# Optimization experiments

Hardware: AMD Instinct MI355X
Metric: run time of the kernel (lower is better)

The kernel has to match this reference:

```python
import jax, jax.numpy as jnp
import numpy as np

N = 50000      # nodes
E = 800000     # edges (before self-loops)
F_IN = 128     # num_features
HID = 32       # hidden_channels
HEADS = 4
CLS = 40       # num_classes
NEG_SLOPE = 0.2


def setup_inputs() -> dict:
    key = jax.random.key(0)
    ks = jax.random.split(key, 10)
    s = 0.1
    x = jax.random.normal(ks[0], (N, F_IN), jnp.float32)
    edge_index = jax.random.randint(ks[1], (2, E), 0, N, jnp.int32)
    W1 = jax.random.normal(ks[2], (F_IN, HEADS * HID), jnp.float32) * s
    att_src1 = jax.random.normal(ks[3], (HEADS, HID), jnp.float32) * s
    att_dst1 = jax.random.normal(ks[4], (HEADS, HID), jnp.float32) * s
    b1 = jnp.zeros((HEADS * HID,), jnp.float32)
    W2 = jax.random.normal(ks[5], (HEADS * HID, CLS), jnp.float32) * s
    att_src2 = jax.random.normal(ks[6], (1, CLS), jnp.float32) * s
    att_dst2 = jax.random.normal(ks[7], (1, CLS), jnp.float32) * s
    b2 = jnp.zeros((CLS,), jnp.float32)
    return {"x": x, "edge_index": edge_index,
            "W1": W1, "att_src1": att_src1, "att_dst1": att_dst1, "b1": b1,
            "W2": W2, "att_src2": att_src2, "att_dst2": att_dst2, "b2": b2}


def gat_layer(x, src, dst, W, a_src, a_dst, b, concat):
    """PyG GATConv: per-head linear, edge attention logits a_src.h_j + a_dst.h_i,
    LeakyReLU, segment softmax over incoming edges per dst, weighted scatter-sum."""
    n = x.shape[0]
    H, C = a_src.shape
    h = (x @ W).reshape(n, H, C)                       # [N, H, C]
    al_s = jnp.einsum('nhc,hc->nh', h, a_src)          # [N, H]
    al_d = jnp.einsum('nhc,hc->nh', h, a_dst)          # [N, H]
    e = jax.nn.leaky_relu(al_s[src] + al_d[dst], NEG_SLOPE)  # [E, H]
    e_max = jax.lax.stop_gradient(jax.ops.segment_max(e, dst, num_segments=n))
    e = jnp.exp(e - e_max[dst])
    denom = jax.ops.segment_sum(e, dst, num_segments=n)      # [N, H]
    alpha = e / (denom[dst] + 1e-16)                         # [E, H]
    out = jax.ops.segment_sum(h[src] * alpha[:, :, None], dst, num_segments=n)  # [N, H, C]
    out = out.reshape(n, H * C) if concat else out.mean(axis=1)
    return out + b


def reference(x, edge_index, W1, att_src1, att_dst1, b1, W2, att_src2, att_dst2, b2):
    n = x.shape[0]
    loops = jnp.arange(n, dtype=edge_index.dtype)
    src = jnp.concatenate([edge_index[0], loops])  # PyG adds self-loops by default
    dst = jnp.concatenate([edge_index[1], loops])
    h = gat_layer(x, src, dst, W1, att_src1, att_dst1, b1, concat=True)
    h = jax.nn.relu(h)  # dropout is identity in eval mode
    h = gat_layer(h, src, dst, W2, att_src2, att_dst2, b2, concat=False)
    return jax.nn.log_softmax(h, axis=1)
```

## Files before the change

kernel.cpp:

```cpp
#include <hip/hip_runtime.h>
#include <hip/hip_bf16.h>
#include <cstdint>
#include <cstddef>

#define NN 50000
#define EE 800000
#define ETOT (EE + NN)
#define FIN 128
#define D1 128
#define HEADS 4
#define HID 32
#define CLS 40
#define NEG 0.2f
#define MAXDEG 64
#define NPART 8
#define PSIZE 6250
#define GB 104
#define BGB (NPART * GB)

typedef __attribute__((ext_vector_type(8))) short short8;
typedef __attribute__((ext_vector_type(4))) float float4v;

union U16 { uint4 u; short8 s; };

__device__ __forceinline__ float bf2f(unsigned short u) {
    union { unsigned int i; float f; } v; v.i = ((unsigned int)u) << 16; return v.f;
}
__device__ __forceinline__ unsigned short f2bf(float f) {
    union { unsigned int i; float f; } v; v.f = f;
    unsigned int r = v.i + 0x7fffu + ((v.i >> 16) & 1u);
    return (unsigned short)(r >> 16);
}

__global__ __launch_bounds__(256, 4) void bg_k(const int* __restrict__ eidx,
                                               int* __restrict__ cnt,
                                               unsigned short* __restrict__ ssrcp,
                                               const float* __restrict__ X,
                                               const float* __restrict__ W,
                                               const float* __restrict__ as1,
                                               const float* __restrict__ ad1,
                                               unsigned int* __restrict__ H1b,
                                               float* __restrict__ ALS1,
                                               float* __restrict__ ALD1) {
    __shared__ uint4 Wl[2048];
    __shared__ float sas[128], sad[128];
    int t = threadIdx.x;

    if (blockIdx.x < BGB) {
        int part = blockIdx.x & (NPART - 1);
        int g    = blockIdx.x >> 3;
        int lo = part * PSIZE, hi = lo + PSIZE;
        int stride = GB * 256;
        for (int i = g * 256 + t; i < ETOT; i += stride) {
            int dN = (i < EE) ? eidx[EE + i] : (i - EE);
            if (dN >= lo && dN < hi) {
                int sN = (i < EE) ? eidx[i] : dN;
                int slot = atomicAdd(&cnt[dN], 1);
                if (slot < MAXDEG) ssrcp[dN * MAXDEG + slot] = (unsigned short)sN;
            }
        }
        return;
    }

    int bI = blockIdx.x - BGB;
    if (t < 128) { sas[t] = as1[t]; sad[t] = ad1[t]; }
    for (int g = t; g < 2048; g += 256) {
        int ct = g >> 8, rem = g & 255, kc = rem >> 6, l = rem & 63;
        int c = ct * 16 + (l & 15);
        int k0 = kc * 32 + (l >> 4) * 8;
        U16 u;
#pragma unroll
        for (int j = 0; j < 8; j++) u.s[j] = (short)f2bf(W[(k0 + j) * D1 + c]);
        Wl[g] = u.u;
    }
    __syncthreads();

    int wid = t >> 6, lane = t & 63, quad = lane >> 4, lrow = lane & 15;
    int wrow0 = bI * 128 + wid * 32;

    short8 afr[2][4];
#pragma unroll
    for (int rt = 0; rt < 2; rt++) {
        int r = wrow0 + rt * 16 + lrow;
#pragma unroll
        for (int kc = 0; kc < 4; kc++) {
            short8 a = {0, 0, 0, 0, 0, 0, 0, 0};
            if (r < NN) {
                const float* xp = X + (size_t)r * FIN + kc * 32 + quad * 8;
                float4 x0 = *(const float4*)xp;
                float4 x1 = *(const float4*)(xp + 4);
                a[0] = (short)f2bf(x0.x); a[1] = (short)f2bf(x0.y);
                a[2] = (short)f2bf(x0.z); a[3] = (short)f2bf(x0.w);
                a[4] = (short)f2bf(x1.x); a[5] = (short)f2bf(x1.y);
                a[6] = (short)f2bf(x1.z); a[7] = (short)f2bf(x1.w);
            }
            afr[rt][kc] = a;
        }
    }

    float4v acc[2][4];

    for (int cp = 0; cp < 2; ++cp) {
#pragma unroll
        for (int rt = 0; rt < 2; rt++)
#pragma unroll
            for (int c4 = 0; c4 < 4; c4++) acc[rt][c4] = (float4v)(0.f);

#pragma unroll
        for (int c4 = 0; c4 < 4; c4++) {
#pragma unroll
            for (int kc = 0; kc < 4; kc++) {
                U16 b; b.u = Wl[((cp * 4 + c4) * 4 + kc) * 64 + lane];
                acc[0][c4] = __builtin_amdgcn_mfma_f32_16x16x32_bf16(afr[0][kc], b.s, acc[0][c4], 0, 0, 0);
                acc[1][c4] = __builtin_amdgcn_mfma_f32_16x16x32_bf16(afr[1][kc], b.s, acc[1][c4], 0, 0, 0);
            }
        }

#pragma unroll
        for (int rt = 0; rt < 2; rt++) {
#pragma unroll
            for (int reg = 0; reg < 4; reg++) {
                float ps[2] = {0.f, 0.f};
                float pd[2] = {0.f, 0.f};
#pragma unroll
                for (int c4 = 0; c4 < 4; c4++) {
                    float v = acc[rt][c4][reg];
                    int ct = cp * 4 + c4;
                    ps[c4 >> 1] += v * sas[ct * 16 + lrow];
                    pd[c4 >> 1] += v * sad[ct * 16 + lrow];
                }
#pragma unroll
                for (int o = 1; o < 16; o <<= 1) {
#pragma unroll
                    for (int h = 0; h < 2; h++) {
                        ps[h] += __shfl_xor(ps[h], o);
                        pd[h] += __shfl_xor(pd[h], o);
                    }
                }
                int r = wrow0 + rt * 16 + quad * 4 + reg;
                if (lrow == 0 && r < NN) {
                    *(float2*)&ALS1[(size_t)r * 4 + cp * 2] = make_float2(ps[0], ps[1]);
                    *(float2*)&ALD1[(size_t)r * 4 + cp * 2] = make_float2(pd[0], pd[1]);
                }
            }
        }

#pragma unroll
        for (int rt = 0; rt < 2; rt++)
#pragma unroll
            for (int c4 = 0; c4 < 4; c4++)
#pragma unroll
                for (int reg = 0; reg < 4; reg++) {
                    float v = acc[rt][c4][reg];
                    float o = __shfl_xor(v, 1);
                    int r = wrow0 + rt * 16 + quad * 4 + reg;
                    if (((lane & 1) == 0) && r < NN) {
                        unsigned int u = (unsigned int)f2bf(v) | ((unsigned int)f2bf(o) << 16);
                        H1b[(size_t)r * 64 + (cp * 4 + c4) * 8 + (lrow >> 1)] = u;
                    }
                }
    }
}

__global__ __launch_bounds__(256) void gather1_k(const int* __restrict__ cnt,
                                                 const unsigned short* __restrict__ ssrcp,
                                                 const uint4* __restrict__ H1b4,
                                                 const float4* __restrict__ ALS,
                                                 const float4* __restrict__ ALD,
                                                 const float* __restrict__ b1,
                                                 uint4* __restrict__ OUT1b4) {
    __shared__ float wlds[4][MAXDEG][4];
    __shared__ int sidlds[4][MAXDEG];
    int wid = threadIdx.x >> 6, lane = threadIdx.x & 63;
    int v = blockIdx.x * 4 + wid;
    int deg = min(cnt[v], MAXDEG);
    float4 ad = ALD[v];
    float w0 = 0.f, w1 = 0.f, w2 = 0.f, w3 = 0.f;
    if (lane < deg) {
        int s = (int)ssrcp[v * MAXDEG + lane];
        sidlds[wid][lane] = s;
        float4 as = ALS[s];
        float l0 = as.x + ad.x; l0 = l0 > 0.f ? l0 : NEG * l0;
        float l1 = as.y + ad.y; l1 = l1 > 0.f ? l1 : NEG * l1;
        float l2 = as.z + ad.z; l2 = l2 > 0.f ? l2 : NEG * l2;
        float l3 = as.w + ad.w; l3 = l3 > 0.f ? l3 : NEG * l3;
        w0 = __expf(l0); w1 = __expf(l1); w2 = __expf(l2); w3 = __expf(l3);
        wlds[wid][lane][0] = w0; wlds[wid][lane][1] = w1;
        wlds[wid][lane][2] = w2; wlds[wid][lane][3] = w3;
    }
    float d0 = w0, d1 = w1, d2 = w2, d3 = w3;
#pragma unroll
    for (int o = 1; o < 64; o <<= 1) {
        d0 += __shfl_xor(d0, o); d1 += __shfl_xor(d1, o);
        d2 += __shfl_xor(d2, o); d3 += __shfl_xor(d3, o);
    }
    __syncthreads();
    int g = lane >> 4, l = lane & 15, head = l >> 2;
    float a0=0.f,a1=0.f,a2=0.f,a3=0.f,a4=0.f,a5=0.f,a6=0.f,a7=0.f;
    for (int j = g; j < deg; j += 4) {
        float wj = wlds[wid][j][head];
        int s = sidlds[wid][j];
        uint4 q = H1b4[(size_t)s * 16 + l];
        a0 += wj * bf2f((unsigned short)(q.x & 0xffffu));
        a1 += wj * bf2f((unsigned short)(q.x >> 16));
        a2 += wj * bf2f((unsigned short)(q.y & 0xffffu));
        a3 += wj * bf2f((unsigned short)(q.y >> 16));
        a4 += wj * bf2f((unsigned short)(q.z & 0xffffu));
        a5 += wj * bf2f((unsigned short)(q.z >> 16));
        a6 += wj * bf2f((unsigned short)(q.w & 0xffffu));
        a7 += wj * bf2f((unsigned short)(q.w >> 16));
    }
#pragma unroll
    for (int o = 16; o < 64; o <<= 1) {
        a0 += __shfl_xor(a0, o); a1 += __shfl_xor(a1, o);
        a2 += __shfl_xor(a2, o); a3 += __shfl_xor(a3, o);
        a4 += __shfl_xor(a4, o); a5 += __shfl_xor(a5, o);
        a6 += __shfl_xor(a6, o); a7 += __shfl_xor(a7, o);
    }
    if (lane < 16) {
        float den = (head == 0) ? d0 : (head == 1) ? d1 : (head == 2) ? d2 : d3;
        den += 1e-16f;
        float4 bA = *(const float4*)&b1[8 * l];
        float4 bB = *(const float4*)&b1[8 * l + 4];
        float o0 = fmaxf(a0 / den + bA.x, 0.f);
        float o1 = fmaxf(a1 / den + bA.y, 0.f);
        float o2 = fmaxf(a2 / den + bA.z, 0.f);
        float o3 = fmaxf(a3 / den + bA.w, 0.f);
        float o4 = fmaxf(a4 / den + bB.x, 0.f);
        float o5 = fmaxf(a5 / den + bB.y, 0.f);
        float o6 = fmaxf(a6 / den + bB.z, 0.f);
        float o7 = fmaxf(a7 / den + bB.w, 0.f);
        uint4 u;
        u.x = (unsigned int)f2bf(o0) | ((unsigned int)f2bf(o1) << 16);
        u.y = (unsigned int)f2bf(o2) | ((unsigned int)f2bf(o3) << 16);
        u.z = (unsigned int)f2bf(o4) | ((unsigned int)f2bf(o5) << 16);
        u.w = (unsigned int)f2bf(o6) | ((unsigned int)f2bf(o7) << 16);
        OUT1b4[(size_t)v * 16 + l] = u;
    }
}

__global__ __launch_bounds__(256) void gemm2_k(const unsigned int* __restrict__ OUT1b,
                                               const float* __restrict__ W2,
                                               const float* __restrict__ as2,
                                               const float* __restrict__ ad2,
                                               unsigned int* __restrict__ H2b,
                                               float* __restrict__ ALS2,
                                               float* __restrict__ ALD2) {
    __shared__ uint4 Wl[768];
    __shared__ float sas[48], sad[48];
    int t = threadIdx.x;
    if (t < 48) {
        sas[t] = (t < CLS) ? as2[t] : 0.f;
        sad[t] = (t < CLS) ? ad2[t] : 0.f;
    }
    for (int g = t; g < 768; g += 256) {
        int ct = g >> 8, rem = g & 255, kc = rem >> 6, l = rem & 63;
        int c = ct * 16 + (l & 15);
        int k0 = kc * 32 + (l >> 4) * 8;
        U16 u;
#pragma unroll
        for (int j = 0; j < 8; j++)
            u.s[j] = (c < CLS) ? (short)f2bf(W2[(k0 + j) * CLS + c]) : (short)0;
        Wl[g] = u.u;
    }
    __syncthreads();

    int wid = t >> 6, lane = t & 63, quad = lane >> 4, lrow = lane & 15;
    int wrow0 = blockIdx.x * 128 + wid * 32;

    U16 afr[2][4];
#pragma unroll
    for (int rt = 0; rt < 2; rt++) {
        int r = wrow0 + rt * 16 + lrow;
#pragma unroll
        for (int kc = 0; kc < 4; kc++) {
            if (r < NN)
                afr[rt][kc].u = ((const uint4*)OUT1b)[(size_t)r * 16 + kc * 4 + quad];
            else
                afr[rt][kc].u = make_uint4(0, 0, 0, 0);
        }
    }

    float4v acc[2][3];
#pragma unroll
    for (int rt = 0; rt < 2; rt++)
#pragma unroll
        for (int ct = 0; ct < 3; ct++) acc[rt][ct] = (float4v)(0.f);

#pragma unroll
    for (int ct = 0; ct < 3; ct++) {
#pragma unroll
        for (int kc = 0; kc < 4; kc++) {
            U16 b; b.u = Wl[(ct * 4 + kc) * 64 + lane];
            acc[0][ct] = __builtin_amdgcn_mfma_f32_16x16x32_bf16(afr[0][kc].s, b.s, acc[0][ct], 0, 0, 0);
            acc[1][ct] = __builtin_amdgcn_mfma_f32_16x16x32_bf16(afr[1][kc].s, b.s, acc[1][ct], 0, 0, 0);
        }
    }

#pragma unroll
    for (int rt = 0; rt < 2; rt++) {
#pragma unroll
        for (int reg = 0; reg < 4; reg++) {
            float ps = 0.f, pd = 0.f;
#pragma unroll
            for (int ct = 0; ct < 3; ct++) {
                float v = acc[rt][ct][reg];
                ps += v * sas[ct * 16 + lrow];
                pd += v * sad[ct * 16 + lrow];
            }
#pragma unroll
            for (int o = 1; o < 16; o <<= 1) {
                ps += __shfl_xor(ps, o);
                pd += __shfl_xor(pd, o);
            }
            int r = wrow0 + rt * 16 + quad * 4 + reg;
            if (lrow == 0 && r < NN) {
                ALS2[r] = ps;
                ALD2[r] = pd;
            }
        }
    }

#pragma unroll
    for (int rt = 0; rt < 2; rt++)
#pragma unroll
        for (int ct = 0; ct < 3; ct++)
#pragma unroll
            for (int reg = 0; reg < 4; reg++) {
                float v = acc[rt][ct][reg];
                float o = __shfl_xor(v, 1);
                int r = wrow0 + rt * 16 + quad * 4 + reg;
                int c = ct * 16 + lrow;
                if (((lane & 1) == 0) && c < CLS && r < NN) {
                    unsigned int u = (unsigned int)f2bf(v) | ((unsigned int)f2bf(o) << 16);
                    H2b[(size_t)r * 20 + (c >> 1)] = u;
                }
            }
}

__global__ __launch_bounds__(256) void gather2_k(const int* __restrict__ cnt,
                                                 const unsigned short* __restrict__ ssrcp,
                                                 const unsigned int* __restrict__ H2b,
                                                 const float* __restrict__ ALS,
                                                 const float* __restrict__ ALD,
                                                 const float* __restrict__ b2,
                                                 float* __restrict__ out) {
    int wid = threadIdx.x >> 6, t = threadIdx.x & 63;
    int v = blockIdx.x * 4 + wid;
    int deg = min(cnt[v], MAXDEG);
    __shared__ float w[4][MAXDEG];
    __shared__ int sid[4][MAXDEG];
    __shared__ float part[4][2][CLS];
    float den = 0.f;
    float adv = ALD[v];
    if (t < deg) {
        int s = (int)ssrcp[(size_t)v * MAXDEG + t];
        sid[wid][t] = s;
        float l = ALS[s] + adv; l = l > 0.f ? l : NEG * l;
        float e = __expf(l);
        w[wid][t] = e; den = e;
    }
    __syncthreads();
    int g = t >> 5, c = t & 31;
    if (c < 20) {
        float ax = 0.f, ay = 0.f;
        for (int j = g; j < deg; j += 2) {
            float wj = w[wid][j];
            unsigned int u = H2b[(size_t)sid[wid][j] * 20 + c];
            ax += wj * bf2f((unsigned short)(u & 0xffffu));
            ay += wj * bf2f((unsigned short)(u >> 16));
        }
        part[wid][g][2 * c] = ax;
        part[wid][g][2 * c + 1] = ay;
    }
#pragma unroll
    for (int o = 32; o > 0; o >>= 1) den += __shfl_xor(den, o);
    __syncthreads();
    float z = (t < CLS) ? (part[wid][0][t] + part[wid][1][t]) / (den + 1e-16f) + b2[t] : -1e30f;
    float mx = z;
#pragma unroll
    for (int o = 32; o > 0; o >>= 1) mx = fmaxf(mx, __shfl_xor(mx, o));
    float ex = (t < CLS) ? __expf(z - mx) : 0.f;
    float se = ex;
#pragma unroll
    for (int o = 32; o > 0; o >>= 1) se += __shfl_xor(se, o);
    if (t < CLS) out[(size_t)v * CLS + t] = z - mx - __logf(se);
}

extern "C" void kernel_launch(void* const* d_in, const int* in_sizes, int n_in,
                              void* d_out, int out_size, void* d_ws, size_t ws_size,
                              hipStream_t stream) {
    const float* x   = (const float*)d_in[0];
    const int*   eix = (const int*)d_in[1];
    const float* W1  = (const float*)d_in[2];
    const float* as1 = (const float*)d_in[3];
    const float* ad1 = (const float*)d_in[4];
    const float* b1  = (const float*)d_in[5];
    const float* W2  = (const float*)d_in[6];
    const float* as2 = (const float*)d_in[7];
    const float* ad2 = (const float*)d_in[8];
    const float* b2  = (const float*)d_in[9];
    float* out = (float*)d_out;

    char* p = (char*)d_ws;
    auto carve = [&](size_t bytes) -> void* {
        void* r = (void*)p;
        p += (bytes + 255) & ~(size_t)255;
        return r;
    };
    unsigned int* H1b   = (unsigned int*)carve((size_t)NN * 64 * 4);
    unsigned int* OUT1b = (unsigned int*)carve((size_t)NN * 64 * 4);
    unsigned int* H2b   = (unsigned int*)carve((size_t)NN * 20 * 4);
    float* ALS1 = (float*)carve((size_t)NN * 4 * 4);
    float* ALD1 = (float*)carve((size_t)NN * 4 * 4);
    float* ALS2 = (float*)carve((size_t)NN * 4);
    float* ALD2 = (float*)carve((size_t)NN * 4);
    int* cnt    = (int*)carve((size_t)NN * 4);
    unsigned short* ssrcp = (unsigned short*)carve((size_t)NN * MAXDEG * 2);

    hipMemsetAsync(cnt, 0, (size_t)NN * 4, stream);

    int gemmBlocks = (NN + 127) / 128;
    bg_k<<<BGB + gemmBlocks, 256, 0, stream>>>(eix, cnt, ssrcp, x, W1, as1, ad1,
                                               H1b, ALS1, ALD1);
    gather1_k<<<NN / 4, 256, 0, stream>>>(cnt, ssrcp, (const uint4*)H1b,
                                          (const float4*)ALS1, (const float4*)ALD1,
                                          b1, (uint4*)OUT1b);
    gemm2_k<<<(NN + 127) / 128, 256, 0, stream>>>(OUT1b, W2, as2, ad2, H2b, ALS2, ALD2);
    gather2_k<<<NN / 4, 256, 0, stream>>>(cnt, ssrcp, H2b, ALS2, ALD2, b2, out);
}
```

Measured before the change: 226.1 us.

## Vectorize edge binning, software-pipeline gathers, widen layer-2 gather lanes

The edge-binning blocks now insert self-loops in a separate pass and read destination indices as int4, which removes the per-element branch on i<EE. The bucket block count also drops from 104 to 79 per partition. Both gather loops are software-pipelined so the next neighbor's row load is issued before the current one is accumulated, hiding gather latency. The layer-2 gather uses 60 of 64 lanes as 3 groups instead of 40 as 2, at the cost of an extra partial-sum slot and integer divide/mod.

Result: faster. 219.4 us (-3.0%).

```diff
diff --git a/kernel.cpp b/kernel.cpp
--- a/kernel.cpp
+++ b/kernel.cpp
@@ -15,7 +15,7 @@
 #define MAXDEG 64
 #define NPART 8
 #define PSIZE 6250
-#define GB 104
+#define GB 79
 #define BGB (NPART * GB)
 
 typedef __attribute__((ext_vector_type(8))) short short8;
@@ -51,12 +51,33 @@
         int g    = blockIdx.x >> 3;
         int lo = part * PSIZE, hi = lo + PSIZE;
         int stride = GB * 256;
-        for (int i = g * 256 + t; i < ETOT; i += stride) {
-            int dN = (i < EE) ? eidx[EE + i] : (i - EE);
-            if (dN >= lo && dN < hi) {
-                int sN = (i < EE) ? eidx[i] : dN;
-                int slot = atomicAdd(&cnt[dN], 1);
-                if (slot < MAXDEG) ssrcp[dN * MAXDEG + slot] = (unsigned short)sN;
+        for (int n = lo + g * 256 + t; n < hi; n += stride) {
+            int slot = atomicAdd(&cnt[n], 1);
+            if (slot < MAXDEG) ssrcp[n * MAXDEG + slot] = (unsigned short)n;
+        }
+        const int4* dst4 = (const int4*)(eidx + EE);
+        for (int i4 = g * 256 + t; i4 < EE / 4; i4 += stride) {
+            int4 d = dst4[i4];
+            int base = i4 * 4;
+            if (d.x >= lo && d.x < hi) {
+                int sN = eidx[base];
+                int slot = atomicAdd(&cnt[d.x], 1);
+                if (slot < MAXDEG) ssrcp[d.x * MAXDEG + slot] = (unsigned short)sN;
+            }
+            if (d.y >= lo && d.y < hi) {
+                int sN = eidx[base + 1];
+                int slot = atomicAdd(&cnt[d.y], 1);
+                if (slot < MAXDEG) ssrcp[d.y * MAXDEG + slot] = (unsigned short)sN;
+            }
+            if (d.z >= lo && d.z < hi) {
+                int sN = eidx[base + 2];
+                int slot = atomicAdd(&cnt[d.z], 1);
+                if (slot < MAXDEG) ssrcp[d.z * MAXDEG + slot] = (unsigned short)sN;
+            }
+            if (d.w >= lo && d.w < hi) {
+                int sN = eidx[base + 3];
+                int slot = atomicAdd(&cnt[d.w], 1);
+                if (slot < MAXDEG) ssrcp[d.w * MAXDEG + slot] = (unsigned short)sN;
             }
         }
         return;
@@ -197,18 +218,32 @@
     __syncthreads();
     int g = lane >> 4, l = lane & 15, head = l >> 2;
     float a0=0.f,a1=0.f,a2=0.f,a3=0.f,a4=0.f,a5=0.f,a6=0.f,a7=0.f;
-    for (int j = g; j < deg; j += 4) {
-        float wj = wlds[wid][j][head];
-        int s = sidlds[wid][j];
-        uint4 q = H1b4[(size_t)s * 16 + l];
-        a0 += wj * bf2f((unsigned short)(q.x & 0xffffu));
-        a1 += wj * bf2f((unsigned short)(q.x >> 16));
-        a2 += wj * bf2f((unsigned short)(q.y & 0xffffu));
-        a3 += wj * bf2f((unsigned short)(q.y >> 16));
-        a4 += wj * bf2f((unsigned short)(q.z & 0xffffu));
-        a5 += wj * bf2f((unsigned short)(q.z >> 16));
-        a6 += wj * bf2f((unsigned short)(q.w & 0xffffu));
-        a7 += wj * bf2f((unsigned short)(q.w >> 16));
+    {
+        int j = g;
+        bool valid = j < deg;
+        float wj = 0.f; uint4 q = {};
+        if (valid) {
+            wj = wlds[wid][j][head];
+            q = H1b4[(size_t)sidlds[wid][j] * 16 + l];
+        }
+        while (valid) {
+            int jn = j + 4;
+            bool vn = jn < deg;
+            float wn = 0.f; uint4 qn = {};
+            if (vn) {
+                wn = wlds[wid][jn][head];
+                qn = H1b4[(size_t)sidlds[wid][jn] * 16 + l];
+            }
+            a0 += wj * bf2f((unsigned short)(q.x & 0xffffu));
+            a1 += wj * bf2f((unsigned short)(q.x >> 16));
+            a2 += wj * bf2f((unsigned short)(q.y & 0xffffu));
+            a3 += wj * bf2f((unsigned short)(q.y >> 16));
+            a4 += wj * bf2f((unsigned short)(q.z & 0xffffu));
+            a5 += wj * bf2f((unsigned short)(q.z >> 16));
+            a6 += wj * bf2f((unsigned short)(q.w & 0xffffu));
+            a7 += wj * bf2f((unsigned short)(q.w >> 16));
+            j = jn; valid = vn; wj = wn; q = qn;
+        }
     }
 #pragma unroll
     for (int o = 16; o < 64; o <<= 1) {
@@ -350,7 +385,7 @@
     int deg = min(cnt[v], MAXDEG);
     __shared__ float w[4][MAXDEG];
     __shared__ int sid[4][MAXDEG];
-    __shared__ float part[4][2][CLS];
+    __shared__ float part[4][3][CLS];
     float den = 0.f;
     float adv = ALD[v];
     if (t < deg) {
@@ -361,14 +396,21 @@
         w[wid][t] = e; den = e;
     }
     __syncthreads();
-    int g = t >> 5, c = t & 31;
-    if (c < 20) {
+    int g = t / 20, c = t % 20;
+    if (t < 60) {
         float ax = 0.f, ay = 0.f;
-        for (int j = g; j < deg; j += 2) {
-            float wj = w[wid][j];
-            unsigned int u = H2b[(size_t)sid[wid][j] * 20 + c];
+        int j = g;
+        bool valid = j < deg;
+        float wj = 0.f; unsigned int u = 0u;
+        if (valid) { wj = w[wid][j]; u = H2b[(size_t)sid[wid][j] * 20 + c]; }
+        while (valid) {
+            int jn = j + 3;
+            bool vn = jn < deg;
+            float wn = 0.f; unsigned int un = 0u;
+            if (vn) { wn = w[wid][jn]; un = H2b[(size_t)sid[wid][jn] * 20 + c]; }
             ax += wj * bf2f((unsigned short)(u & 0xffffu));
             ay += wj * bf2f((unsigned short)(u >> 16));
+            j = jn; valid = vn; wj = wn; u = un;
         }
         part[wid][g][2 * c] = ax;
         part[wid][g][2 * c + 1] = ay;
@@ -376,7 +418,8 @@
 #pragma unroll
     for (int o = 32; o > 0; o >>= 1) den += __shfl_xor(den, o);
     __syncthreads();
-    float z = (t < CLS) ? (part[wid][0][t] + part[wid][1][t]) / (den + 1e-16f) + b2[t] : -1e30f;
+    float z = (t < CLS) ? (part[wid][0][t] + part[wid][1][t] + part[wid][2][t]) / (den + 1e-16f) + b2[t]
+                        : -1e30f;
     float mx = z;
 #pragma unroll
     for (int o = 32; o > 0; o >>= 1) mx = fmaxf(mx, __shfl_xor(mx, o));
```
